# Optimization experiments

Hardware: AMD Instinct MI355X
Metric: run time of the kernel (lower is better)

## Reference

```python
import jax, jax.numpy as jnp
import numpy as np

N_NODES = 50000
N_EDGES = 1_600_000
F_IN = 128
HIDDEN = 128
N_REL = 8
N_GRAPHS = 64


def setup_inputs() -> dict:
    key = jax.random.key(0)
    ks = jax.random.split(key, 16)
    x = jax.random.normal(ks[0], (N_NODES, F_IN), dtype=jnp.float32)
    edge_index = jax.random.randint(ks[1], (2, N_EDGES), 0, N_NODES, dtype=jnp.int32)
    edge_type = jax.random.randint(ks[2], (N_EDGES,), 0, N_REL, dtype=jnp.int32)
    edge_attr = jax.nn.one_hot(edge_type, N_REL, dtype=jnp.float32)  # one-hot relation encoding
    batch = jnp.sort(jax.random.randint(ks[3], (N_NODES,), 0, N_GRAPHS, dtype=jnp.int32))
    s = 1.0 / np.sqrt(F_IN)
    params = {}
    dims = [(F_IN, HIDDEN), (HIDDEN, HIDDEN), (HIDDEN, HIDDEN)]
    for i, (fi, fo) in enumerate(dims, 1):
        params[f"W{i}"] = jax.random.normal(ks[3 + 3 * i], (N_REL, fi, fo), dtype=jnp.float32) * s
        params[f"root{i}"] = jax.random.normal(ks[4 + 3 * i], (fi, fo), dtype=jnp.float32) * s
        params[f"b{i}"] = jnp.zeros((fo,), dtype=jnp.float32)
    lin_w = jax.random.normal(ks[13], (HIDDEN, HIDDEN), dtype=jnp.float32) * (1.0 / np.sqrt(HIDDEN))
    lin_b = jnp.zeros((HIDDEN,), dtype=jnp.float32)
    return {"x": x, "edge_index": edge_index, "edge_attr": edge_attr, "batch": batch,
            **params, "lin_w": lin_w, "lin_b": lin_b}


def _rgcn_conv(x, src, dst, edge_type, W, root, bias):
    # PyG RGCNConv with aggr='mean': per-relation mean of transformed neighbors + root + bias.
    # Mean is linear, so aggregate raw features per (dst, relation) then apply W_r.
    n = x.shape[0]
    seg = dst * N_REL + edge_type                      # combined segment id [E]
    msg = x[src]                                       # [E, F_in] gather
    agg = jax.ops.segment_sum(msg, seg, num_segments=n * N_REL)
    cnt = jax.ops.segment_sum(jnp.ones((src.shape[0],), x.dtype), seg, num_segments=n * N_REL)
    agg = agg / jnp.maximum(cnt, 1.0)[:, None]
    agg = agg.reshape(n, N_REL, -1)                    # [N, R, F_in]
    return jnp.einsum('nri,rio->no', agg, W) + x @ root + bias


def reference(x, edge_index, edge_attr, batch,
              W1, root1, b1, W2, root2, b2, W3, root3, b3, lin_w, lin_b):
    src, dst = edge_index[0], edge_index[1]
    edge_type = jnp.argmax(edge_attr, axis=1)          # np.where(edge_attr == 1)[1]
    h = jax.nn.relu(_rgcn_conv(x, src, dst, edge_type, W1, root1, b1))
    h = jax.nn.relu(_rgcn_conv(h, src, dst, edge_type, W2, root2, b2))
    h = jax.nn.relu(_rgcn_conv(h, src, dst, edge_type, W3, root3, b3))
    # global_mean_pool over graphs
    sums = jax.ops.segment_sum(h, batch, num_segments=N_GRAPHS)
    cnts = jax.ops.segment_sum(jnp.ones((h.shape[0],), h.dtype), batch, num_segments=N_GRAPHS)
    pooled = sums / jnp.maximum(cnts, 1.0)[:, None]    # [G, hidden]
    return pooled @ lin_w + lin_b
```

## Files before the change

### kernel.cpp

```cpp
#include <hip/hip_runtime.h>
#include <hip/hip_fp16.h>

#define N_NODESC 50000
#define N_EDGESC 1600000
#define FEAT 128
#define NREL 8
#define NSEG (N_NODESC * NREL)
#define NGRAPH 64
#define NKC 36
#define WPACK_ELEMS (NKC * 4 * 128 * 8)
#define WPACK_BLKS (WPACK_ELEMS / 256)
#define NHALF (N_NODESC * FEAT)
#define CVT_BLKS ((NHALF / 4 + 255) / 256)

typedef float f32x4 __attribute__((ext_vector_type(4)));
typedef _Float16 f16x8 __attribute__((ext_vector_type(8)));
typedef unsigned int u32x2 __attribute__((ext_vector_type(2)));
typedef unsigned int u32x4 __attribute__((ext_vector_type(4)));

static inline size_t align256(size_t x) { return (x + 255) & ~(size_t)255; }

__device__ __forceinline__ float4 h4tof4(u32x2 r) {
  const __half* h = (const __half*)&r;
  return make_float4(__half2float(h[0]), __half2float(h[1]),
                     __half2float(h[2]), __half2float(h[3]));
}

__global__ void k_zero(int* __restrict__ p, int n) {
  int i = blockIdx.x * blockDim.x + threadIdx.x;
  int stride = gridDim.x * blockDim.x;
  for (; i < n; i += stride) p[i] = 0;
}

__global__ void k_edge_hist(const int* __restrict__ ei, const float* __restrict__ eattr,
                            int* __restrict__ seg, int* __restrict__ cnt) {
  int e = blockIdx.x * blockDim.x + threadIdx.x;
  if (e >= N_EDGESC) return;
  int dst = ei[N_EDGESC + e];
  const float4* ap = (const float4*)(eattr + (size_t)e * 8);
  float4 a0 = ap[0], a1 = ap[1];
  int ty = 0;
  if (a0.y > 0.5f) ty = 1;
  if (a0.z > 0.5f) ty = 2;
  if (a0.w > 0.5f) ty = 3;
  if (a1.x > 0.5f) ty = 4;
  if (a1.y > 0.5f) ty = 5;
  if (a1.z > 0.5f) ty = 6;
  if (a1.w > 0.5f) ty = 7;
  int s = dst * NREL + ty;
  seg[e] = s;
  atomicAdd(&cnt[s], 1);
}

__global__ void k_scan1(const int* __restrict__ cnt, int* __restrict__ outIncl,
                        int* __restrict__ bsums, int n) {
  __shared__ int sd[256];
  int t = threadIdx.x;
  int base = blockIdx.x * 4096 + t * 16;
  int v[16];
  int s = 0;
#pragma unroll
  for (int j = 0; j < 16; ++j) {
    int idx = base + j;
    int x = (idx < n) ? cnt[idx] : 0;
    s += x;
    v[j] = s;
  }
  sd[t] = s;
  __syncthreads();
  for (int off = 1; off < 256; off <<= 1) {
    int add = (t >= off) ? sd[t - off] : 0;
    __syncthreads();
    sd[t] += add;
    __syncthreads();
  }
  int prev = (t > 0) ? sd[t - 1] : 0;
#pragma unroll
  for (int j = 0; j < 16; ++j) {
    int idx = base + j;
    if (idx < n) outIncl[idx] = prev + v[j];
  }
  if (t == 255) bsums[blockIdx.x] = sd[255];
}

__global__ void k_scan2(int* __restrict__ bsums, int nb) {
  __shared__ int sd[128];
  int t = threadIdx.x;
  int v = (t < nb) ? bsums[t] : 0;
  sd[t] = v;
  __syncthreads();
  for (int off = 1; off < 128; off <<= 1) {
    int add = (t >= off) ? sd[t - off] : 0;
    __syncthreads();
    sd[t] += add;
    __syncthreads();
  }
  if (t < nb) bsums[t] = sd[t] - v;
}

__global__ void k_scan3(int* __restrict__ offsets, const int* __restrict__ bsums, int n) {
  int i = blockIdx.x * blockDim.x + threadIdx.x;
  if (i == 0) offsets[0] = 0;
  if (i < n) offsets[i + 1] += bsums[i >> 12];
}

__global__ void k_scatter(const int* __restrict__ ei, const int* __restrict__ seg,
                          const int* __restrict__ offsets, int* __restrict__ cursor,
                          int* __restrict__ ssrc) {
  int e = blockIdx.x * blockDim.x + threadIdx.x;
  if (e >= N_EDGESC) return;
  int s = seg[e];
  int p = offsets[s] + atomicAdd(&cursor[s], 1);
  ssrc[p] = ei[e];
}

__global__ void k_prep(const float* __restrict__ W1, const float* __restrict__ r1,
                       const float* __restrict__ W2, const float* __restrict__ r2,
                       const float* __restrict__ W3, const float* __restrict__ r3,
                       const float* __restrict__ x,
                       __half* __restrict__ whi3, __half* __restrict__ wlo3,
                       __half* __restrict__ p0) {
  int b = blockIdx.x;
  if (b < 3 * WPACK_BLKS) {
    int L = b / WPACK_BLKS;
    int idx = (b - L * WPACK_BLKS) * 256 + threadIdx.x;
    const float* W = (L == 0) ? W1 : (L == 1) ? W2 : W3;
    const float* root = (L == 0) ? r1 : (L == 1) ? r2 : r3;
    int j = idx & 7;
    int n = (idx >> 3) & 127;
    int slot = idx >> 10;
    int k = slot * 8 + j;
    float v = (k < 1024) ? W[(size_t)k * 128 + n] : root[(size_t)(k - 1024) * 128 + n];
    __half hi = __float2half(v);
    float lof = v - __half2float(hi);
    whi3[(size_t)L * WPACK_ELEMS + idx] = hi;
    wlo3[(size_t)L * WPACK_ELEMS + idx] = __float2half(lof);
  } else {
    int i = (b - 3 * WPACK_BLKS) * 256 + threadIdx.x;
    if (i * 4 < NHALF) {
      float4 v = *(const float4*)&x[i * 4];
      __half h[4] = {__float2half(v.x), __float2half(v.y),
                     __float2half(v.z), __float2half(v.w)};
      *(uint2*)&p0[(size_t)i * 4] = *(uint2*)h;
    }
  }
}

__global__ __launch_bounds__(256, 8) void k_agg(
    const __half* __restrict__ in, const int* __restrict__ offsets,
    const int* __restrict__ ssrc, __half* __restrict__ agg,
    int nodeBase, int nodeCount) {
  int t = blockIdx.x * blockDim.x + threadIdx.x;
  int un = t >> 5;
  int l = t & 31;
  if (un >= nodeCount) return;
  int node = nodeBase + un;
  for (int r = 0; r < NREL; ++r) {
    int sidx = node * NREL + r;
    int beg = offsets[sidx], end = offsets[sidx + 1];
    float4 s = make_float4(0.f, 0.f, 0.f, 0.f);
    for (int base = beg; base < end; base += 4) {
      int last = end - 1;
      int e1 = base + 1 <= last ? base + 1 : last;
      int e2 = base + 2 <= last ? base + 2 : last;
      int e3 = base + 3 <= last ? base + 3 : last;
      int i0 = ssrc[base], i1 = ssrc[e1], i2 = ssrc[e2], i3 = ssrc[e3];
      u32x2 r0 = *(const u32x2*)&in[(size_t)i0 * FEAT + l * 4];
      u32x2 r1 = *(const u32x2*)&in[(size_t)i1 * FEAT + l * 4];
      u32x2 r2 = *(const u32x2*)&in[(size_t)i2 * FEAT + l * 4];
      u32x2 r3 = *(const u32x2*)&in[(size_t)i3 * FEAT + l * 4];
      float4 v0 = h4tof4(r0), v1 = h4tof4(r1), v2 = h4tof4(r2), v3 = h4tof4(r3);
      s.x += v0.x; s.y += v0.y; s.z += v0.z; s.w += v0.w;
      if (base + 1 < end) { s.x += v1.x; s.y += v1.y; s.z += v1.z; s.w += v1.w; }
      if (base + 2 < end) { s.x += v2.x; s.y += v2.y; s.z += v2.z; s.w += v2.w; }
      if (base + 3 < end) { s.x += v3.x; s.y += v3.y; s.z += v3.z; s.w += v3.w; }
    }
    int c = end - beg;
    if (c > 1) {
      float inv = 1.0f / (float)c;
      s.x *= inv; s.y *= inv; s.z *= inv; s.w *= inv;
    }
    __half hv[4] = {__float2half(s.x), __float2half(s.y), __float2half(s.z), __float2half(s.w)};
    __builtin_nontemporal_store(*(u32x2*)hv,
                                (u32x2*)&agg[((size_t)un * NREL + r) * FEAT + l * 4]);
  }
}

__global__ __launch_bounds__(256, 3) void k_gemm_mfma(
    const __half* __restrict__ aggc,
    const __half* __restrict__ xin,
    const __half* __restrict__ Whi, const __half* __restrict__ Wlo,
    const float* __restrict__ bias, __half* __restrict__ out16,
    int n0g, int rows) {
  __shared__ __half Ah[2][4096] __attribute__((aligned(16)));
  __shared__ __half Bh[2][4096] __attribute__((aligned(16)));
  __shared__ __half Bl[2][4096] __attribute__((aligned(16)));

  const int t = threadIdx.x;
  const int lane = t & 63, wave = t >> 6;
  const int l15 = lane & 15, lg = lane >> 4;
  const int wrow0 = wave * 32;
  const int m0 = blockIdx.x * 128;
  const int srow = t >> 1, half = t & 1;

  int rowc = srow;
  if (m0 + rowc >= rows) rowc = rows - 1 - m0;
  if (rowc < 0) rowc = 0;
  const __half* aggRow = aggc + (size_t)(m0 + rowc) * 1024 + half * 16;
  const __half* xRow = xin + (size_t)(n0g + m0 + rowc) * FEAT + half * 16;

  u32x4 av0, av1, sbh0, sbh1, sbl0, sbl1;

#define LOADC(kc)                                                          \
  {                                                                        \
    const __half* asrc = ((kc) < 32) ? (aggRow + (kc) * 32)                \
                                     : (xRow + ((kc) - 32) * 32);          \
    av0 = ((const u32x4*)asrc)[0];                                         \
    av1 = ((const u32x4*)asrc)[1];                                         \
    const u32x4* bhs = (const u32x4*)(Whi + (size_t)(kc) * 4096);          \
    const u32x4* bls = (const u32x4*)(Wlo + (size_t)(kc) * 4096);          \
    sbh0 = bhs[t * 2]; sbh1 = bhs[t * 2 + 1];                              \
    sbl0 = bls[t * 2]; sbl1 = bls[t * 2 + 1];                              \
  }
#define WRITEC(b)                                                          \
  {                                                                        \
    int g0 = half * 2;                                                     \
    *(u32x4*)&Ah[b][(g0 * 128 + srow) * 8] = av0;                          \
    *(u32x4*)&Ah[b][((g0 + 1) * 128 + srow) * 8] = av1;                    \
    ((u32x4*)Bh[b])[t * 2] = sbh0; ((u32x4*)Bh[b])[t * 2 + 1] = sbh1;      \
    ((u32x4*)Bl[b])[t * 2] = sbl0; ((u32x4*)Bl[b])[t * 2 + 1] = sbl1;      \
  }

  f32x4 acc[2][8];
#pragma unroll
  for (int a = 0; a < 2; ++a)
#pragma unroll
    for (int b = 0; b < 8; ++b) acc[a][b] = (f32x4){0.f, 0.f, 0.f, 0.f};

  LOADC(0);
  WRITEC(0);
  LOADC(1);
  __syncthreads();

  for (int kc = 0; kc < NKC; ++kc) {
    const int cur = kc & 1;
    f16x8 af[2];
#pragma unroll
    for (int mf = 0; mf < 2; ++mf) {
      int ar = wrow0 + mf * 16 + l15;
      af[mf] = *(const f16x8*)&Ah[cur][(lg * 128 + ar) * 8];
    }
#pragma unroll
    for (int nf = 0; nf < 8; ++nf) {
      int bn = nf * 16 + l15;
      f16x8 vh = *(const f16x8*)&Bh[cur][(lg * 128 + bn) * 8];
      f16x8 vl = *(const f16x8*)&Bl[cur][(lg * 128 + bn) * 8];
      acc[0][nf] = __builtin_amdgcn_mfma_f32_16x16x32_f16(af[0], vh, acc[0][nf], 0, 0, 0);
      acc[0][nf] = __builtin_amdgcn_mfma_f32_16x16x32_f16(af[0], vl, acc[0][nf], 0, 0, 0);
      acc[1][nf] = __builtin_amdgcn_mfma_f32_16x16x32_f16(af[1], vh, acc[1][nf], 0, 0, 0);
      acc[1][nf] = __builtin_amdgcn_mfma_f32_16x16x32_f16(af[1], vl, acc[1][nf], 0, 0, 0);
    }
    if (kc < NKC - 1) {
      WRITEC(cur ^ 1);
      if (kc < NKC - 2) LOADC(kc + 2);
      __syncthreads();
    }
  }
#undef LOADC
#undef WRITEC

  float bcol[8];
#pragma unroll
  for (int nf = 0; nf < 8; ++nf) bcol[nf] = bias[nf * 16 + l15];
#pragma unroll
  for (int mf = 0; mf < 2; ++mf)
#pragma unroll
    for (int nf = 0; nf < 8; ++nf)
#pragma unroll
      for (int j = 0; j < 4; ++j) {
        int grow = m0 + wrow0 + mf * 16 + lg * 4 + j;
        if (grow < rows) {
          float v = acc[mf][nf][j] + bcol[nf];
          v = v > 0.f ? v : 0.f;
          out16[(size_t)(n0g + grow) * FEAT + nf * 16 + l15] = __float2half(v);
        }
      }
}

__global__ void k_pool(const __half* __restrict__ h, const int* __restrict__ batch,
                       const float* __restrict__ lw, const float* __restrict__ lb,
                       float* __restrict__ out) {
  __shared__ float sums[8][128];
  __shared__ float prow[128];
  int gidx = blockIdx.x, t = threadIdx.x;
  int f = t & 127, grp = t >> 7;
  int lo = 0, hi = N_NODESC;
  while (lo < hi) {
    int mid = (lo + hi) >> 1;
    if (batch[mid] < gidx) lo = mid + 1; else hi = mid;
  }
  int start = lo;
  hi = N_NODESC;
  while (lo < hi) {
    int mid = (lo + hi) >> 1;
    if (batch[mid] < gidx + 1) lo = mid + 1; else hi = mid;
  }
  int end = lo;
  float s = 0.f;
  for (int n = start + grp; n < end; n += 8) s += __half2float(h[(size_t)n * FEAT + f]);
  sums[grp][f] = s;
  __syncthreads();
  if (grp == 0) {
    float tot = 0.f;
#pragma unroll
    for (int gg = 0; gg < 8; ++gg) tot += sums[gg][f];
    int c = end - start;
    prow[f] = (c > 0) ? tot / (float)c : 0.f;
  }
  __syncthreads();
  float a = 0.f;
  for (int k = grp * 16; k < grp * 16 + 16; ++k) a = fmaf(prow[k], lw[(size_t)k * FEAT + f], a);
  __syncthreads();
  sums[grp][f] = a;
  __syncthreads();
  if (grp == 0) {
    float tot = lb[f];
#pragma unroll
    for (int gg = 0; gg < 8; ++gg) tot += sums[gg][f];
    out[(size_t)gidx * FEAT + f] = tot;
  }
}

extern "C" void kernel_launch(void* const* d_in, const int* in_sizes, int n_in,
                              void* d_out, int out_size, void* d_ws, size_t ws_size,
                              hipStream_t stream) {
  const float* x = (const float*)d_in[0];
  const int* ei = (const int*)d_in[1];
  const float* eattr = (const float*)d_in[2];
  const int* batch = (const int*)d_in[3];
  const float* Wl[3] = {(const float*)d_in[4], (const float*)d_in[7], (const float*)d_in[10]};
  const float* rl[3] = {(const float*)d_in[5], (const float*)d_in[8], (const float*)d_in[11]};
  const float* bl[3] = {(const float*)d_in[6], (const float*)d_in[9], (const float*)d_in[12]};
  const float* lw = (const float*)d_in[13];
  const float* lb = (const float*)d_in[14];
  float* out = (float*)d_out;
  (void)n_in; (void)in_sizes; (void)out_size;

  size_t pos = 0;
  char* base = (char*)d_ws;
  auto alloc = [&](size_t bytes) { char* q = base + pos; pos += align256(bytes); return q; };
  int* seg = (int*)alloc(sizeof(int) * (size_t)N_EDGESC);
  int* cntcur = (int*)alloc(sizeof(int) * (size_t)2 * NSEG);
  int* cnt = cntcur;
  int* cursor = cntcur + NSEG;
  int* offsets = (int*)alloc(sizeof(int) * (size_t)(NSEG + 1));
  int* bsums = (int*)alloc(sizeof(int) * 1024);
  int* ssrc = (int*)alloc(sizeof(int) * (size_t)N_EDGESC);
  __half* p0 = (__half*)alloc(sizeof(__half) * (size_t)NHALF);
  __half* p1 = (__half*)alloc(sizeof(__half) * (size_t)NHALF);
  __half* whi3 = (__half*)alloc(sizeof(__half) * (size_t)3 * WPACK_ELEMS);
  __half* wlo3 = (__half*)alloc(sizeof(__half) * (size_t)3 * WPACK_ELEMS);
  size_t remain = (ws_size > pos) ? (ws_size - pos) : 0;
  long long cn = (long long)(remain / (sizeof(__half) * NREL * FEAT));
  int chunkNodes = (cn > N_NODESC) ? N_NODESC : (int)cn;
  chunkNodes &= ~127;
  if (chunkNodes < 128) chunkNodes = 128;
  __half* aggbuf = (__half*)(base + pos);
  int nchunks = (N_NODESC + chunkNodes - 1) / chunkNodes;

  hipLaunchKernelGGL(k_zero, dim3(2048), dim3(256), 0, stream, cntcur, 2 * NSEG);
  hipLaunchKernelGGL(k_edge_hist, dim3((N_EDGESC + 255) / 256), dim3(256), 0, stream,
                     ei, eattr, seg, cnt);
  int nbScan = (NSEG + 4095) / 4096;
  hipLaunchKernelGGL(k_scan1, dim3(nbScan), dim3(256), 0, stream, cnt, offsets + 1, bsums, NSEG);
  hipLaunchKernelGGL(k_scan2, dim3(1), dim3(128), 0, stream, bsums, nbScan);
  hipLaunchKernelGGL(k_scan3, dim3((NSEG + 255) / 256), dim3(256), 0, stream, offsets, bsums, NSEG);
  hipLaunchKernelGGL(k_scatter, dim3((N_EDGESC + 255) / 256), dim3(256), 0, stream,
                     ei, seg, offsets, cursor, ssrc);

  hipLaunchKernelGGL(k_prep, dim3(3 * WPACK_BLKS + CVT_BLKS), dim3(256), 0, stream,
                     Wl[0], rl[0], Wl[1], rl[1], Wl[2], rl[2], x, whi3, wlo3, p0);

  const __half* inPtr = p0;
  __half* outPtr = p1;
  for (int L = 0; L < 3; ++L) {
    const __half* whi = whi3 + (size_t)L * WPACK_ELEMS;
    const __half* wlo = wlo3 + (size_t)L * WPACK_ELEMS;
    for (int c = 0; c < nchunks; ++c) {
      int nodeBase = c * chunkNodes;
      int rowsC = N_NODESC - nodeBase;
      if (rowsC > chunkNodes) rowsC = chunkNodes;
      int aggBlocks = (rowsC * 32 + 255) / 256;
      hipLaunchKernelGGL(k_agg, dim3(aggBlocks), dim3(256), 0, stream,
                         inPtr, offsets, ssrc, aggbuf, nodeBase, rowsC);
      hipLaunchKernelGGL(k_gemm_mfma, dim3((rowsC + 127) / 128), dim3(256), 0, stream,
                         aggbuf, inPtr, whi, wlo, bl[L], outPtr, nodeBase, rowsC);
    }
    const __half* tmp = inPtr;
    inPtr = outPtr;
    outPtr = (__half*)tmp;
  }

  hipLaunchKernelGGL(k_pool, dim3(NGRAPH), dim3(1024), 0, stream, p1, batch, lw, lb, out);
}
```

Before: 751.2 us.

## Split GEMM tile along N and stage weights via global_load_lds

Each GEMM block now covers 128 rows by 64 output columns instead of 128, which doubles the grid and halves the weight LDS buffers and accumulators, so the launch bound rises to four blocks per CU. Weight chunks are copied straight from global memory into LDS with global_load_lds rather than through registers. This aims for more parallelism and occupancy and shorter register-to-LDS staging. In exchange, each A tile (aggregated features) is loaded twice from global memory, once per column half.

```diff
diff --git a/kernel.cpp b/kernel.cpp
--- a/kernel.cpp
+++ b/kernel.cpp
@@ -24,6 +24,12 @@
   const __half* h = (const __half*)&r;
   return make_float4(__half2float(h[0]), __half2float(h[1]),
                      __half2float(h[2]), __half2float(h[3]));
+}
+
+__device__ __forceinline__ void gll16(const void* g, void* l) {
+  __builtin_amdgcn_global_load_lds(
+      (const __attribute__((address_space(1))) unsigned int*)g,
+      (__attribute__((address_space(3))) unsigned int*)l, 16, 0, 0);
 }
 
 __global__ void k_zero(int* __restrict__ p, int n) {
@@ -186,21 +192,23 @@
   }
 }
 
-__global__ __launch_bounds__(256, 3) void k_gemm_mfma(
+__global__ __launch_bounds__(256, 4) void k_gemm_mfma(
     const __half* __restrict__ aggc,
     const __half* __restrict__ xin,
     const __half* __restrict__ Whi, const __half* __restrict__ Wlo,
     const float* __restrict__ bias, __half* __restrict__ out16,
     int n0g, int rows) {
   __shared__ __half Ah[2][4096] __attribute__((aligned(16)));
-  __shared__ __half Bh[2][4096] __attribute__((aligned(16)));
-  __shared__ __half Bl[2][4096] __attribute__((aligned(16)));
+  __shared__ __half Bh[2][2048] __attribute__((aligned(16)));
+  __shared__ __half Bl[2][2048] __attribute__((aligned(16)));
 
   const int t = threadIdx.x;
   const int lane = t & 63, wave = t >> 6;
   const int l15 = lane & 15, lg = lane >> 4;
   const int wrow0 = wave * 32;
-  const int m0 = blockIdx.x * 128;
+  const int tileM = blockIdx.x >> 1, h = blockIdx.x & 1;
+  const int m0 = tileM * 128;
+  const int col0 = h * 64;
   const int srow = t >> 1, half = t & 1;
 
   int rowc = srow;
@@ -209,80 +217,83 @@
   const __half* aggRow = aggc + (size_t)(m0 + rowc) * 1024 + half * 16;
   const __half* xRow = xin + (size_t)(n0g + m0 + rowc) * FEAT + half * 16;
 
-  u32x4 av0, av1, sbh0, sbh1, sbl0, sbl1;
-
-#define LOADC(kc)                                                          \
+  const char* whiB = (const char*)Whi + (size_t)wave * 2048 + (size_t)h * 1024 +
+                     (size_t)lane * 16;
+  const char* wloB = (const char*)Wlo + (size_t)wave * 2048 + (size_t)h * 1024 +
+                     (size_t)lane * 16;
+
+#define STAGE_B(kc, b)                                                     \
+  {                                                                        \
+    gll16(whiB + (size_t)(kc) * 8192, (char*)&Bh[b][0] + wave * 1024);     \
+    gll16(wloB + (size_t)(kc) * 8192, (char*)&Bl[b][0] + wave * 1024);     \
+  }
+#define LOADA(kc)                                                          \
   {                                                                        \
     const __half* asrc = ((kc) < 32) ? (aggRow + (kc) * 32)                \
                                      : (xRow + ((kc) - 32) * 32);          \
     av0 = ((const u32x4*)asrc)[0];                                         \
     av1 = ((const u32x4*)asrc)[1];                                         \
-    const u32x4* bhs = (const u32x4*)(Whi + (size_t)(kc) * 4096);          \
-    const u32x4* bls = (const u32x4*)(Wlo + (size_t)(kc) * 4096);          \
-    sbh0 = bhs[t * 2]; sbh1 = bhs[t * 2 + 1];                              \
-    sbl0 = bls[t * 2]; sbl1 = bls[t * 2 + 1];                              \
-  }
-#define WRITEC(b)                                                          \
+  }
+#define WRITEA(b)                                                          \
   {                                                                        \
     int g0 = half * 2;                                                     \
     *(u32x4*)&Ah[b][(g0 * 128 + srow) * 8] = av0;                          \
     *(u32x4*)&Ah[b][((g0 + 1) * 128 + srow) * 8] = av1;                    \
-    ((u32x4*)Bh[b])[t * 2] = sbh0; ((u32x4*)Bh[b])[t * 2 + 1] = sbh1;      \
-    ((u32x4*)Bl[b])[t * 2] = sbl0; ((u32x4*)Bl[b])[t * 2 + 1] = sbl1;      \
-  }
-
-  f32x4 acc[2][8];
+  }
+
+  f32x4 acc[2][4];
 #pragma unroll
   for (int a = 0; a < 2; ++a)
 #pragma unroll
-    for (int b = 0; b < 8; ++b) acc[a][b] = (f32x4){0.f, 0.f, 0.f, 0.f};
-
-  LOADC(0);
-  WRITEC(0);
-  LOADC(1);
+    for (int b = 0; b < 4; ++b) acc[a][b] = (f32x4){0.f, 0.f, 0.f, 0.f};
+
+  u32x4 av0, av1;
+
+  STAGE_B(0, 0);
+  LOADA(0);
+  WRITEA(0);
+  LOADA(1);
   __syncthreads();
 
   for (int kc = 0; kc < NKC; ++kc) {
     const int cur = kc & 1;
-    f16x8 af[2];
-#pragma unroll
-    for (int mf = 0; mf < 2; ++mf) {
-      int ar = wrow0 + mf * 16 + l15;
-      af[mf] = *(const f16x8*)&Ah[cur][(lg * 128 + ar) * 8];
-    }
-#pragma unroll
-    for (int nf = 0; nf < 8; ++nf) {
+    if (kc < NKC - 1) STAGE_B(kc + 1, cur ^ 1);
+    f16x8 af0 = *(const f16x8*)&Ah[cur][(lg * 128 + wrow0 + l15) * 8];
+    f16x8 af1 = *(const f16x8*)&Ah[cur][(lg * 128 + wrow0 + 16 + l15) * 8];
+#pragma unroll
+    for (int nf = 0; nf < 4; ++nf) {
       int bn = nf * 16 + l15;
-      f16x8 vh = *(const f16x8*)&Bh[cur][(lg * 128 + bn) * 8];
-      f16x8 vl = *(const f16x8*)&Bl[cur][(lg * 128 + bn) * 8];
-      acc[0][nf] = __builtin_amdgcn_mfma_f32_16x16x32_f16(af[0], vh, acc[0][nf], 0, 0, 0);
-      acc[0][nf] = __builtin_amdgcn_mfma_f32_16x16x32_f16(af[0], vl, acc[0][nf], 0, 0, 0);
-      acc[1][nf] = __builtin_amdgcn_mfma_f32_16x16x32_f16(af[1], vh, acc[1][nf], 0, 0, 0);
-      acc[1][nf] = __builtin_amdgcn_mfma_f32_16x16x32_f16(af[1], vl, acc[1][nf], 0, 0, 0);
+      f16x8 vh = *(const f16x8*)&Bh[cur][(lg * 64 + bn) * 8];
+      f16x8 vl = *(const f16x8*)&Bl[cur][(lg * 64 + bn) * 8];
+      acc[0][nf] = __builtin_amdgcn_mfma_f32_16x16x32_f16(af0, vh, acc[0][nf], 0, 0, 0);
+      acc[0][nf] = __builtin_amdgcn_mfma_f32_16x16x32_f16(af0, vl, acc[0][nf], 0, 0, 0);
+      acc[1][nf] = __builtin_amdgcn_mfma_f32_16x16x32_f16(af1, vh, acc[1][nf], 0, 0, 0);
+      acc[1][nf] = __builtin_amdgcn_mfma_f32_16x16x32_f16(af1, vl, acc[1][nf], 0, 0, 0);
     }
     if (kc < NKC - 1) {
-      WRITEC(cur ^ 1);
-      if (kc < NKC - 2) LOADC(kc + 2);
+      WRITEA(cur ^ 1);
+      if (kc < NKC - 2) LOADA(kc + 2);
       __syncthreads();
     }
   }
-#undef LOADC
-#undef WRITEC
-
-  float bcol[8];
-#pragma unroll
-  for (int nf = 0; nf < 8; ++nf) bcol[nf] = bias[nf * 16 + l15];
+#undef STAGE_B
+#undef LOADA
+#undef WRITEA
+
+  float bcol[4];
+#pragma unroll
+  for (int nf = 0; nf < 4; ++nf) bcol[nf] = bias[col0 + nf * 16 + l15];
 #pragma unroll
   for (int mf = 0; mf < 2; ++mf)
 #pragma unroll
-    for (int nf = 0; nf < 8; ++nf)
+    for (int nf = 0; nf < 4; ++nf)
 #pragma unroll
       for (int j = 0; j < 4; ++j) {
         int grow = m0 + wrow0 + mf * 16 + lg * 4 + j;
         if (grow < rows) {
           float v = acc[mf][nf][j] + bcol[nf];
           v = v > 0.f ? v : 0.f;
-          out16[(size_t)(n0g + grow) * FEAT + nf * 16 + l15] = __float2half(v);
+          out16[(size_t)(n0g + grow) * FEAT + col0 + nf * 16 + l15] = __float2half(v);
         }
       }
 }
@@ -393,7 +404,8 @@
       int aggBlocks = (rowsC * 32 + 255) / 256;
       hipLaunchKernelGGL(k_agg, dim3(aggBlocks), dim3(256), 0, stream,
                          inPtr, offsets, ssrc, aggbuf, nodeBase, rowsC);
-      hipLaunchKernelGGL(k_gemm_mfma, dim3((rowsC + 127) / 128), dim3(256), 0, stream,
+      int nTilesM = (rowsC + 127) / 128;
+      hipLaunchKernelGGL(k_gemm_mfma, dim3(nTilesM * 2), dim3(256), 0, stream,
                          aggbuf, inPtr, whi, wlo, bl[L], outPtr, nodeBase, rowsC);
     }
     const __half* tmp = inPtr;
```

After: 817.3 us. 1.09x slower.
